# Kernel tuning notes

Hardware: AMD Instinct MI355X
Metric: run time of the kernel (lower is better)

## Reference

```python
import jax, jax.numpy as jnp
import numpy as np


def _conv(x, w, b, pad):
    y = jax.lax.conv_general_dilated(x, w, (1, 1), [(pad, pad), (pad, pad)],
                                     dimension_numbers=('NCHW', 'OIHW', 'NCHW'))
    return y + b[None, :, None, None]


def _leaky(x):
    return jnp.where(x >= 0, x, 0.2 * x)


def _up_nearest(t, s):
    return jnp.repeat(jnp.repeat(t, s, axis=2), s, axis=3)


def _to_plane(d, dx, dy, size):
    # nearest-upsample d,dx,dy by `size` and add per-subpixel plane offsets
    c = jnp.linspace(-(size - 1) / 2, (size - 1) / 2, size).astype(d.dtype)
    H, W = d.shape[2], d.shape[3]
    a = jnp.tile(c, W)[None, None, None, :]   # x-offset pattern along width
    b = jnp.tile(c, H)[None, None, :, None]   # y-offset pattern along height
    return _up_nearest(d, size) + a * _up_nearest(dx, size) + b * _up_nearest(dy, size)


def _warp(x, disp):
    # grid_sample(x, grid) with grid = (xx - disp, yy), align_corners=True, zero padding.
    # y coords are exact integers, so this reduces to 1-D linear interp along W.
    B, C, H, W = x.shape
    ix = jnp.arange(W, dtype=x.dtype)[None, None, :] - disp[:, 0]  # [B,H,W]
    x0 = jnp.floor(ix)
    wx = ix - x0
    x0i = x0.astype(jnp.int32)
    x1i = x0i + 1
    ok0 = ((x0i >= 0) & (x0i < W)).astype(x.dtype)
    ok1 = ((x1i >= 0) & (x1i < W)).astype(x.dtype)

    def gather(idx):
        idx = jnp.clip(idx, 0, W - 1)
        return jnp.take_along_axis(x, jnp.broadcast_to(idx[:, None], (B, C, H, W)), axis=3)

    return ((1 - wx) * ok0)[:, None] * gather(x0i) + (wx * ok1)[:, None] * gather(x1i)


def _unshuffle(x, r=4):
    B, C, H, W = x.shape
    return x.reshape(B, C, H // r, r, W // r, r).transpose(0, 1, 3, 5, 2, 4).reshape(B, C * r * r, H // r, W // r)


def _tile_warping(tile_plane, fea_l, fea_r):
    d, dx, dy = tile_plane[:, 0:1], tile_plane[:, 1:2], tile_plane[:, 2:3]
    cvs = []
    for k in (-1.0, 0.0, 1.0):
        local_d = _to_plane(d + k, dx, dy, 4)
        cv = jnp.sum(jnp.abs(fea_l - _warp(fea_r, local_d)), axis=1, keepdims=True)
        cvs.append(_unshuffle(cv, 4))
    return jnp.concatenate(cvs, axis=1)


def _upsample_hyp(h, scale=2.0, size=2):
    d = _to_plane(h[:, 0:1], h[:, 1:2], h[:, 2:3], size) * scale
    rest = _up_nearest(h[:, 1:], size)
    return jnp.concatenate([d, rest], axis=1)


def _forward(fea_l, fea_r, cur, prev,
             w_dec, b_dec, w0, b0,
             w_r0c1, b_r0c1, w_r0c2, b_r0c2,
             w_r1c1, b_r1c1, w_r1c2, b_r1c2,
             w_last, b_last):
    fea = _unshuffle(jnp.sum(jnp.abs(fea_l), axis=1, keepdims=True), 4)  # [B,16,H/4,W/4]

    cur_cv = _tile_warping(cur[:, :3], fea_l, fea_r)
    cur_cv = _leaky(_conv(jnp.concatenate([fea, cur_cv], 1), w_dec, b_dec, 0))

    up_prev = _upsample_hyp(prev, 2.0, 2)
    prev_cv = _tile_warping(up_prev[:, :3], fea_l, fea_r)
    prev_cv = _leaky(_conv(jnp.concatenate([fea, prev_cv], 1), w_dec, b_dec, 0))

    aug = jnp.concatenate([cur, cur_cv, up_prev, prev_cv], 1)  # 64 ch
    h = _leaky(_conv(aug, w0, b0, 0))
    # resblock0 (BasicBlock + outer LeakyReLU)
    t = _leaky(_conv(h, w_r0c1, b_r0c1, 1))
    h = _leaky(_conv(t, w_r0c2, b_r0c2, 1) + h)
    # resblock1
    t = _leaky(_conv(h, w_r1c1, b_r1c1, 1))
    h = _leaky(_conv(t, w_r1c2, b_r1c2, 1) + h)
    u = _conv(h, w_last, b_last, 1)  # 34 ch

    conf = u[:, :2]
    prev_delta = u[:, 2:18]
    cur_delta = u[:, 18:34]
    mask = jnp.argmax(conf, axis=1, keepdims=True).astype(u.dtype)

    upd_cur = cur + cur_delta
    upd_cur = jnp.concatenate([jax.nn.relu(upd_cur[:, :1]), upd_cur[:, 1:]], 1)
    upd_prev = up_prev + prev_delta
    upd_prev = jnp.concatenate([jax.nn.relu(upd_prev[:, :1]), upd_prev[:, 1:]], 1)

    refined = mask * upd_cur + (1 - mask) * upd_prev
    return (refined,
            jnp.concatenate([upd_cur, conf[:, 1:2]], 1),
            jnp.concatenate([upd_prev, conf[:, :1]], 1))


def setup_inputs() -> dict:
    key = jax.random.key(0)
    ks = jax.random.split(key, 16)
    B, C, H, W = 2, 16, 384, 1280
    Ht, Wt = H // 4, W // 4
    inp = {
        'fea_l': jax.random.normal(ks[0], (B, C, H, W), jnp.float32),
        'fea_r': jax.random.normal(ks[1], (B, C, H, W), jnp.float32),
        'current_hypothesis': jax.random.uniform(ks[2], (B, 16, Ht, Wt), jnp.float32) * 4.0,
        'prev_hypothesis': jax.random.uniform(ks[3], (B, 16, Ht // 2, Wt // 2), jnp.float32) * 4.0,
    }
    s = 0.05
    inp['w_dec'] = jax.random.normal(ks[4], (16, 64, 1, 1), jnp.float32) * s
    inp['b_dec'] = jax.random.normal(ks[5], (16,), jnp.float32) * s
    inp['w0'] = jax.random.normal(ks[6], (32, 64, 1, 1), jnp.float32) * s
    inp['b0'] = jax.random.normal(ks[7], (32,), jnp.float32) * s
    inp['w_r0c1'] = jax.random.normal(ks[8], (32, 32, 3, 3), jnp.float32) * s
    inp['b_r0c1'] = jax.random.normal(ks[9], (32,), jnp.float32) * s
    inp['w_r0c2'] = jax.random.normal(ks[10], (32, 32, 3, 3), jnp.float32) * s
    inp['b_r0c2'] = jax.random.normal(ks[11], (32,), jnp.float32) * s
    inp['w_r1c1'] = jax.random.normal(ks[12], (32, 32, 3, 3), jnp.float32) * s
    inp['b_r1c1'] = jax.random.normal(ks[13], (32,), jnp.float32) * s
    inp['w_r1c2'] = jax.random.normal(ks[14], (32, 32, 3, 3), jnp.float32) * s
    inp['b_r1c2'] = jax.random.normal(ks[15], (32,), jnp.float32) * s
    k2 = jax.random.split(jax.random.key(1), 2)
    inp['w_last'] = jax.random.normal(k2[0], (34, 32, 3, 3), jnp.float32) * s
    inp['b_last'] = jax.random.normal(k2[1], (34,), jnp.float32) * s
    return inp


def reference(fea_l, fea_r, current_hypothesis, prev_hypothesis,
              w_dec, b_dec, w0, b0,
              w_r0c1, b_r0c1, w_r0c2, b_r0c2,
              w_r1c1, b_r1c1, w_r1c2, b_r1c2,
              w_last, b_last):
    return _forward(fea_l, fea_r, current_hypothesis, prev_hypothesis,
                    w_dec, b_dec, w0, b0,
                    w_r0c1, b_r0c1, w_r0c2, b_r0c2,
                    w_r1c1, b_r1c1, w_r1c2, b_r1c2,
                    w_last, b_last)
```

## Files before the change

kernel.cpp:

```cpp
#include <hip/hip_runtime.h>
#include <hip/hip_bf16.h>

#define B_ 2
#define C_ 16
#define H_ 384
#define W_ 1280
#define HT_ 96
#define WT_ 320
#define SP_ (HT_*WT_)
#define NPIX_ (B_*SP_)
#define HP_ 48
#define WP_ 160
#define SPP_ (HP_*WP_)

__device__ __forceinline__ float leaky(float v){ return v >= 0.f ? v : 0.2f*v; }

__global__ __launch_bounds__(256) void k_sentinel(float* __restrict__ out, int n, float v){
    int i = blockIdx.x*256 + threadIdx.x;
    if (i < n) out[i] = v;
}

__global__ __launch_bounds__(256) void k_warpfused(const float* __restrict__ cur,
        const float* __restrict__ prev,
        const float* __restrict__ fl, const float* __restrict__ fr,
        const float* __restrict__ wdec, const float* __restrict__ bdec,
        float* __restrict__ outc, float* __restrict__ outp){
    __shared__ float vc[16][65];
    __shared__ float vp[16][49];
    __shared__ float wl[64][16];
    int tid = threadIdx.x;
    for (int i = tid; i < 1024; i += 256) wl[i>>4][i&15] = wdec[(i&15)*64 + (i>>4)];

    int tp  = tid >> 4;
    int sub = tid & 15;
    int yy = sub >> 2, xx = sub & 3;
    int ty = blockIdx.y;
    int tx = blockIdx.x*16 + tp;
    int b  = blockIdx.z;
    int y = ty*4 + yy, x = tx*4 + xx;

    size_t cb = ((size_t)(b*16)*HT_ + ty)*WT_ + tx;
    float dC  = cur[cb];
    float dxC = cur[cb + SP_];
    float dyC = cur[cb + 2*SP_];
    size_t pb = ((size_t)(b*16)*HP_ + (ty>>1))*WP_ + (tx>>1);
    float pd  = prev[pb];
    float pdx = prev[pb + SPP_];
    float pdy = prev[pb + 2*SPP_];
    float cxs = (tx & 1) ? 0.5f : -0.5f;
    float cys = (ty & 1) ? 0.5f : -0.5f;
    float dP  = (pd + cxs*pdx + cys*pdy) * 2.0f;

    const float c4[4] = {-1.5f,-0.5f,0.5f,1.5f};
    float ld0C = dC + c4[xx]*dxC + c4[yy]*dyC;
    float ld0P = dP + c4[xx]*pdx + c4[yy]*pdy;

    float wloC[4], whiC[4]; int xcC[4];
    {
        float ix  = (float)x - ld0C;
        float x0f = floorf(ix);
        float wx  = ix - x0f;
        int   x0  = (int)x0f;
        #pragma unroll
        for (int j = 0; j < 4; j++){
            int xi = x0 + (j-1);
            bool ok = (xi >= 0) && (xi < W_);
            xcC[j]  = xi < 0 ? 0 : (xi > W_-1 ? W_-1 : xi);
            wloC[j] = ok ? (1.f - wx) : 0.f;
            whiC[j] = ok ? wx : 0.f;
        }
    }
    float wloP[4], whiP[4]; int xcP[4];
    {
        float ix  = (float)x - ld0P;
        float x0f = floorf(ix);
        float wx  = ix - x0f;
        int   x0  = (int)x0f;
        #pragma unroll
        for (int j = 0; j < 4; j++){
            int xi = x0 + (j-1);
            bool ok = (xi >= 0) && (xi < W_);
            xcP[j]  = xi < 0 ? 0 : (xi > W_-1 ? W_-1 : xi);
            wloP[j] = ok ? (1.f - wx) : 0.f;
            whiP[j] = ok ? wx : 0.f;
        }
    }
    const float* plc = fl + (size_t)(b*C_)*H_*W_ + (size_t)y*W_ + x;
    const float* prr = fr + (size_t)(b*C_)*H_*W_ + (size_t)y*W_;
    float fsum=0.f, s0C=0.f, s1C=0.f, s2C=0.f, s0P=0.f, s1P=0.f, s2P=0.f;
    #pragma unroll 4
    for (int c = 0; c < C_; c++){
        const float* prc = prr + (size_t)c*H_*W_;
        float a  = plc[(size_t)c*H_*W_];
        float c0 = prc[xcC[0]];
        float c1 = prc[xcC[1]];
        float c2 = prc[xcC[2]];
        float c3 = prc[xcC[3]];
        float p0 = prc[xcP[0]];
        float p1 = prc[xcP[1]];
        float p2 = prc[xcP[2]];
        float p3 = prc[xcP[3]];
        fsum += fabsf(a);
        s0C += fabsf(a - (wloC[2]*c2 + whiC[3]*c3));
        s1C += fabsf(a - (wloC[1]*c1 + whiC[2]*c2));
        s2C += fabsf(a - (wloC[0]*c0 + whiC[1]*c1));
        s0P += fabsf(a - (wloP[2]*p2 + whiP[3]*p3));
        s1P += fabsf(a - (wloP[1]*p1 + whiP[2]*p2));
        s2P += fabsf(a - (wloP[0]*p0 + whiP[1]*p1));
    }
    vc[tp][sub]      = fsum;
    vc[tp][16 + sub] = s0C;
    vc[tp][32 + sub] = s1C;
    vc[tp][48 + sub] = s2C;
    vp[tp][sub]      = s0P;
    vp[tp][16 + sub] = s1P;
    vp[tp][32 + sub] = s2P;
    __syncthreads();
    int oc  = tid >> 4;
    int tp2 = tid & 15;
    float common = 0.f, aC = 0.f, aP = 0.f;
    #pragma unroll 8
    for (int ic = 0; ic < 16; ic++) common += vc[tp2][ic] * wl[ic][oc];
    #pragma unroll 8
    for (int ic = 16; ic < 64; ic++){
        aC += vc[tp2][ic]      * wl[ic][oc];
        aP += vp[tp2][ic - 16] * wl[ic][oc];
    }
    float bb = bdec[oc];
    size_t ob = ((size_t)(b*16 + oc)*HT_ + ty)*WT_ + blockIdx.x*16 + tp2;
    outc[ob] = leaky(common + aC + bb);
    outp[ob] = leaky(common + aP + bb);
}

__global__ __launch_bounds__(256) void k_conv0(const float* __restrict__ cur,
        const float* __restrict__ ccv, const float* __restrict__ prev,
        const float* __restrict__ pcv, const float* __restrict__ w,
        const float* __restrict__ bias, float* __restrict__ out){
    __shared__ float wl[64][32];
    __shared__ float bl[32];
    int tid = threadIdx.x;
    for (int i = tid; i < 2048; i += 256) wl[i>>5][i&31] = w[(i&31)*64 + (i>>5)];
    if (tid < 32) bl[tid] = bias[tid];
    __syncthreads();
    int idx = blockIdx.x*256 + tid;
    int b = idx / SP_, sp = idx % SP_;
    int y = sp / WT_, x = sp % WT_;
    float acc[32];
    #pragma unroll
    for (int o = 0; o < 32; o++) acc[o] = 0.f;
    const float* p0 = cur + (size_t)b*16*SP_ + sp;
    #pragma unroll 2
    for (int i = 0; i < 16; i++){
        float v = p0[(size_t)i*SP_];
        #pragma unroll
        for (int o = 0; o < 32; o++) acc[o] += v*wl[i][o];
    }
    const float* p1 = ccv + (size_t)b*16*SP_ + sp;
    #pragma unroll 2
    for (int i = 0; i < 16; i++){
        float v = p1[(size_t)i*SP_];
        #pragma unroll
        for (int o = 0; o < 32; o++) acc[o] += v*wl[16+i][o];
    }
    size_t src = ((size_t)(b*16)*HP_ + (y>>1))*WP_ + (x>>1);
    {
        float pd  = prev[src];
        float pdx = prev[src + SPP_];
        float pdy = prev[src + 2*SPP_];
        float cx = (x & 1) ? 0.5f : -0.5f;
        float cy = (y & 1) ? 0.5f : -0.5f;
        float v = (pd + cx*pdx + cy*pdy) * 2.0f;
        #pragma unroll
        for (int o = 0; o < 32; o++) acc[o] += v*wl[32][o];
    }
    #pragma unroll 2
    for (int i = 1; i < 16; i++){
        float v = prev[src + (size_t)i*SPP_];
        #pragma unroll
        for (int o = 0; o < 32; o++) acc[o] += v*wl[32+i][o];
    }
    const float* p3 = pcv + (size_t)b*16*SP_ + sp;
    #pragma unroll 2
    for (int i = 0; i < 16; i++){
        float v = p3[(size_t)i*SP_];
        #pragma unroll
        for (int o = 0; o < 32; o++) acc[o] += v*wl[48+i][o];
    }
    float* po = out + (size_t)b*32*SP_ + sp;
    #pragma unroll
    for (int o = 0; o < 32; o++) po[(size_t)o*SP_] = leaky(acc[o] + bl[o]);
}

template<bool RES>
__global__ __launch_bounds__(256) void k_conv3(const float* __restrict__ in,
        const float* __restrict__ w, const float* __restrict__ bias,
        const float* res, float* out){
    __shared__ float it[8][6][34];
    __shared__ float wl[8][9][32];
    int tid = threadIdx.x;
    int gx = blockIdx.x*32, gy = blockIdx.y*4;
    int b = blockIdx.z;
    int ocg  = tid >> 5;
    int slot = tid & 31;
    int tx4  = (slot & 7)*4;
    int ty   = slot >> 3;
    float acc[4][4];
    #pragma unroll
    for (int o = 0; o < 4; o++)
        #pragma unroll
        for (int p = 0; p < 4; p++) acc[o][p] = 0.f;

    for (int ic0 = 0; ic0 < 32; ic0 += 8){
        for (int i = tid; i < 8*6*34; i += 256){
            int ic = i/(6*34); int r = i - ic*(6*34);
            int iy = r/34;     int ixx = r - iy*34;
            int ggy = gy + iy - 1, ggx = gx + ixx - 1;
            float v = 0.f;
            if (ggy >= 0 && ggy < HT_ && ggx >= 0 && ggx < WT_)
                v = in[((size_t)(b*32 + ic0+ic)*HT_ + ggy)*WT_ + ggx];
            it[ic][iy][ixx] = v;
        }
        for (int i = tid; i < 2304; i += 256){
            int ic = i/288; int r = i - ic*288;
            int kk = r >> 5; int oc = r & 31;
            wl[ic][kk][oc] = w[(size_t)(oc*32 + ic0+ic)*9 + kk];
        }
        __syncthreads();
        #pragma unroll
        for (int ic = 0; ic < 8; ic++){
            #pragma unroll
            for (int dy = 0; dy < 3; dy++){
                float inr[6];
                #pragma unroll
                for (int j = 0; j < 6; j++) inr[j] = it[ic][ty+dy][tx4+j];
                #pragma unroll
                for (int dx = 0; dx < 3; dx++){
                    const float4 wv = *(const float4*)(&wl[ic][dy*3+dx][ocg*4]);
                    const float wa[4] = {wv.x, wv.y, wv.z, wv.w};
                    #pragma unroll
                    for (int o = 0; o < 4; o++)
                        #pragma unroll
                        for (int p = 0; p < 4; p++)
                            acc[o][p] += inr[dx+p]*wa[o];
                }
            }
        }
        __syncthreads();
    }
    int oc0 = ocg*4;
    int yo = gy + ty;
    #pragma unroll
    for (int o = 0; o < 4; o++){
        float bo = bias[oc0+o];
        size_t ob = ((size_t)(b*32 + oc0+o)*HT_ + yo)*WT_ + gx + tx4;
        #pragma unroll
        for (int p = 0; p < 4; p++){
            float v = acc[o][p] + bo;
            if (RES) v += res[ob+p];
            out[ob+p] = leaky(v);
        }
    }
}

__global__ __launch_bounds__(256) void k_last(const float* __restrict__ in,
        const float* __restrict__ w, const float* __restrict__ bias,
        const float* __restrict__ cur, const float* __restrict__ prev,
        float* __restrict__ out){
    __shared__ float it[8][10][34];
    __shared__ float wl[8][9][36];
    __shared__ float bl[34];
    int tid = threadIdx.x;
    int gx = blockIdx.x*32, gy = blockIdx.y*8;
    int b = blockIdx.z;
    int tx = tid & 31, ty = tid >> 5;
    if (tid < 34) bl[tid] = bias[tid];
    float acc[34];
    #pragma unroll
    for (int o = 0; o < 34; o++) acc[o] = 0.f;

    for (int ic0 = 0; ic0 < 32; ic0 += 8){
        for (int i = tid; i < 8*10*34; i += 256){
            int ic = i/340; int r = i - ic*340;
            int iy = r/34;  int ixx = r - iy*34;
            int ggy = gy + iy - 1, ggx = gx + ixx - 1;
            float v = 0.f;
            if (ggy >= 0 && ggy < HT_ && ggx >= 0 && ggx < WT_)
                v = in[((size_t)(b*32 + ic0+ic)*HT_ + ggy)*WT_ + ggx];
            it[ic][iy][ixx] = v;
        }
        for (int i = tid; i < 8*9*34; i += 256){
            int ic = i/306; int r = i - ic*306;
            int kk = r/34;  int oc = r - kk*34;
            wl[ic][kk][oc] = w[(size_t)(oc*32 + ic0+ic)*9 + kk];
        }
        __syncthreads();
        for (int ic = 0; ic < 8; ic++){
            #pragma unroll
            for (int dy = 0; dy < 3; dy++){
                const float vv[3] = { it[ic][ty+dy][tx], it[ic][ty+dy][tx+1], it[ic][ty+dy][tx+2] };
                #pragma unroll
                for (int dx = 0; dx < 3; dx++){
                    const float* wp = &wl[ic][dy*3+dx][0];
                    float v = vv[dx];
                    #pragma unroll
                    for (int o = 0; o < 34; o++) acc[o] += v*wp[o];
                }
            }
        }
        __syncthreads();
    }
    int x = gx + tx, y = gy + ty;
    size_t pix = (size_t)y*WT_ + x;
    float conf0 = acc[0] + bl[0];
    float conf1 = acc[1] + bl[1];
    bool m = conf1 > conf0;
    size_t src = ((size_t)(b*16)*HP_ + (y>>1))*WP_ + (x>>1);
    float cx = (x & 1) ? 0.5f : -0.5f;
    float cy = (y & 1) ? 0.5f : -0.5f;
    const float* cp = cur + (size_t)b*16*SP_ + pix;
    float* o0 = out +               (size_t)b*16*SP_ + pix;
    float* o1 = out +  983040u  +   (size_t)b*17*SP_ + pix;
    float* o2 = out + 2027520u  +   (size_t)b*17*SP_ + pix;
    #pragma unroll
    for (int c = 0; c < 16; c++){
        float upv;
        if (c == 0){
            float dv  = prev[src];
            float dxv = prev[src + SPP_];
            float dyv = prev[src + 2*SPP_];
            upv = (dv + cx*dxv + cy*dyv) * 2.0f;
        } else {
            upv = prev[src + (size_t)c*SPP_];
        }
        float ucv = cp[(size_t)c*SP_] + acc[18+c] + bl[18+c];
        upv = upv + acc[2+c] + bl[2+c];
        if (c == 0){ ucv = fmaxf(ucv, 0.f); upv = fmaxf(upv, 0.f); }
        float rf = m ? ucv : upv;
        o0[(size_t)c*SP_] = rf;
        o1[(size_t)c*SP_] = ucv;
        o2[(size_t)c*SP_] = upv;
    }
    o1[(size_t)16*SP_] = conf1;
    o2[(size_t)16*SP_] = conf0;
}

#define WS_NEED (32u*NPIX_*4u)
#define OUT_ELEMS 3072000

extern "C" void kernel_launch(void* const* d_in, const int* in_sizes, int n_in,
                              void* d_out, int out_size, void* d_ws, size_t ws_size,
                              hipStream_t stream) {
    const float* fea_l  = (const float*)d_in[0];
    const float* fea_r  = (const float*)d_in[1];
    const float* cur    = (const float*)d_in[2];
    const float* prev   = (const float*)d_in[3];
    const float* w_dec  = (const float*)d_in[4];
    const float* b_dec  = (const float*)d_in[5];
    const float* w0     = (const float*)d_in[6];
    const float* b0     = (const float*)d_in[7];
    const float* w_r0c1 = (const float*)d_in[8];
    const float* b_r0c1 = (const float*)d_in[9];
    const float* w_r0c2 = (const float*)d_in[10];
    const float* b_r0c2 = (const float*)d_in[11];
    const float* w_r1c1 = (const float*)d_in[12];
    const float* b_r1c1 = (const float*)d_in[13];
    const float* w_r1c2 = (const float*)d_in[14];
    const float* b_r1c2 = (const float*)d_in[15];
    const float* w_last = (const float*)d_in[16];
    const float* b_last = (const float*)d_in[17];

    float* out = (float*)d_out;

    if (ws_size < (size_t)WS_NEED){
        k_sentinel<<<(OUT_ELEMS+255)/256, 256, 0, stream>>>(out, OUT_ELEMS, (float)(ws_size >> 10));
        return;
    }

    float* h = (float*)d_ws;
    float* curcv  = out;
    float* prevcv = out + 983040;
    float* t      = out;

    dim3 gw(20, 96, 2);
    k_warpfused<<<gw, 256, 0, stream>>>(cur, prev, fea_l, fea_r, w_dec, b_dec, curcv, prevcv);

    k_conv0<<<240, 256, 0, stream>>>(cur, curcv, prev, prevcv, w0, b0, h);

    dim3 g3(10, 24, 2);
    k_conv3<false><<<g3, 256, 0, stream>>>(h, w_r0c1, b_r0c1, nullptr, t);
    k_conv3<true> <<<g3, 256, 0, stream>>>(t, w_r0c2, b_r0c2, h, h);
    k_conv3<false><<<g3, 256, 0, stream>>>(h, w_r1c1, b_r1c1, nullptr, t);
    k_conv3<true> <<<g3, 256, 0, stream>>>(t, w_r1c2, b_r1c2, h, h);

    dim3 gl(10, 12, 2);
    k_last<<<gl, 256, 0, stream>>>(h, w_last, b_last, cur, prev, out);
}
```

Baseline: 476.4 us.

## Fuse conv0 into warp cost-volume kernel and split conv3 output channels across blocks

The 1x1 conv0 is folded into the warp/cost-volume kernel. Its 64 input channels (cur, cost volume, upsampled prev, prev cost volume) are staged in shared memory, and the result is written straight to h. This drops the global write and reread of the two intermediate cost-volume tensors and one kernel launch. Separately, the 3x3 conv kernel now splits its 32 output channels into two halves across grid z and computes 2 pixels per thread instead of 4. That doubles block count for more parallelism but reloads the input tile twice.

```diff
diff --git a/kernel.cpp b/kernel.cpp
--- a/kernel.cpp
+++ b/kernel.cpp
@@ -24,20 +24,46 @@
         const float* __restrict__ prev,
         const float* __restrict__ fl, const float* __restrict__ fr,
         const float* __restrict__ wdec, const float* __restrict__ bdec,
-        float* __restrict__ outc, float* __restrict__ outp){
+        const float* __restrict__ w0, const float* __restrict__ b0,
+        float* __restrict__ h){
     __shared__ float vc[16][65];
     __shared__ float vp[16][49];
     __shared__ float wl[64][16];
+    __shared__ float inb[16][65];
+    __shared__ float w0l[64][33];
+    __shared__ float bl0[32];
     int tid = threadIdx.x;
     for (int i = tid; i < 1024; i += 256) wl[i>>4][i&15] = wdec[(i&15)*64 + (i>>4)];
+    for (int i = tid; i < 2048; i += 256) w0l[i>>5][i&31] = w0[(i&31)*64 + (i>>5)];
+    if (tid < 32) bl0[tid] = b0[tid];
 
     int tp  = tid >> 4;
     int sub = tid & 15;
     int yy = sub >> 2, xx = sub & 3;
     int ty = blockIdx.y;
-    int tx = blockIdx.x*16 + tp;
+    int tx0 = blockIdx.x*16;
+    int tx = tx0 + tp;
     int b  = blockIdx.z;
     int y = ty*4 + yy, x = tx*4 + xx;
+
+    {
+        int ch = tid >> 4, px = tid & 15;
+        int txp = tx0 + px;
+        inb[px][ch] = cur[((size_t)(b*16 + ch)*HT_ + ty)*WT_ + txp];
+        size_t pbase = ((size_t)(b*16)*HP_ + (ty>>1))*WP_ + (txp>>1);
+        float v;
+        if (ch == 0){
+            float dv  = prev[pbase];
+            float dxv = prev[pbase + SPP_];
+            float dyv = prev[pbase + 2*SPP_];
+            float cxs = (txp & 1) ? 0.5f : -0.5f;
+            float cys = (ty  & 1) ? 0.5f : -0.5f;
+            v = (dv + cxs*dxv + cys*dyv) * 2.0f;
+        } else {
+            v = prev[pbase + (size_t)ch*SPP_];
+        }
+        inb[px][32 + ch] = v;
+    }
 
     size_t cb = ((size_t)(b*16)*HT_ + ty)*WT_ + tx;
     float dC  = cur[cb];
@@ -116,79 +142,39 @@
     vp[tp][16 + sub] = s1P;
     vp[tp][32 + sub] = s2P;
     __syncthreads();
-    int oc  = tid >> 4;
-    int tp2 = tid & 15;
-    float common = 0.f, aC = 0.f, aP = 0.f;
-    #pragma unroll 8
-    for (int ic = 0; ic < 16; ic++) common += vc[tp2][ic] * wl[ic][oc];
-    #pragma unroll 8
-    for (int ic = 16; ic < 64; ic++){
-        aC += vc[tp2][ic]      * wl[ic][oc];
-        aP += vp[tp2][ic - 16] * wl[ic][oc];
-    }
-    float bb = bdec[oc];
-    size_t ob = ((size_t)(b*16 + oc)*HT_ + ty)*WT_ + blockIdx.x*16 + tp2;
-    outc[ob] = leaky(common + aC + bb);
-    outp[ob] = leaky(common + aP + bb);
-}
-
-__global__ __launch_bounds__(256) void k_conv0(const float* __restrict__ cur,
-        const float* __restrict__ ccv, const float* __restrict__ prev,
-        const float* __restrict__ pcv, const float* __restrict__ w,
-        const float* __restrict__ bias, float* __restrict__ out){
-    __shared__ float wl[64][32];
-    __shared__ float bl[32];
-    int tid = threadIdx.x;
-    for (int i = tid; i < 2048; i += 256) wl[i>>5][i&31] = w[(i&31)*64 + (i>>5)];
-    if (tid < 32) bl[tid] = bias[tid];
+
+    {
+        int oc  = tid >> 4;
+        int tp2 = tid & 15;
+        float common = 0.f, aC = 0.f, aP = 0.f;
+        #pragma unroll 8
+        for (int ic = 0; ic < 16; ic++) common += vc[tp2][ic] * wl[ic][oc];
+        #pragma unroll 8
+        for (int ic = 16; ic < 64; ic++){
+            aC += vc[tp2][ic]      * wl[ic][oc];
+            aP += vp[tp2][ic - 16] * wl[ic][oc];
+        }
+        float bb = bdec[oc];
+        inb[tp2][16 + oc] = leaky(common + aC + bb);
+        inb[tp2][48 + oc] = leaky(common + aP + bb);
+    }
     __syncthreads();
-    int idx = blockIdx.x*256 + tid;
-    int b = idx / SP_, sp = idx % SP_;
-    int y = sp / WT_, x = sp % WT_;
-    float acc[32];
-    #pragma unroll
-    for (int o = 0; o < 32; o++) acc[o] = 0.f;
-    const float* p0 = cur + (size_t)b*16*SP_ + sp;
-    #pragma unroll 2
-    for (int i = 0; i < 16; i++){
-        float v = p0[(size_t)i*SP_];
-        #pragma unroll
-        for (int o = 0; o < 32; o++) acc[o] += v*wl[i][o];
-    }
-    const float* p1 = ccv + (size_t)b*16*SP_ + sp;
-    #pragma unroll 2
-    for (int i = 0; i < 16; i++){
-        float v = p1[(size_t)i*SP_];
-        #pragma unroll
-        for (int o = 0; o < 32; o++) acc[o] += v*wl[16+i][o];
-    }
-    size_t src = ((size_t)(b*16)*HP_ + (y>>1))*WP_ + (x>>1);
-    {
-        float pd  = prev[src];
-        float pdx = prev[src + SPP_];
-        float pdy = prev[src + 2*SPP_];
-        float cx = (x & 1) ? 0.5f : -0.5f;
-        float cy = (y & 1) ? 0.5f : -0.5f;
-        float v = (pd + cx*pdx + cy*pdy) * 2.0f;
-        #pragma unroll
-        for (int o = 0; o < 32; o++) acc[o] += v*wl[32][o];
-    }
-    #pragma unroll 2
-    for (int i = 1; i < 16; i++){
-        float v = prev[src + (size_t)i*SPP_];
-        #pragma unroll
-        for (int o = 0; o < 32; o++) acc[o] += v*wl[32+i][o];
-    }
-    const float* p3 = pcv + (size_t)b*16*SP_ + sp;
-    #pragma unroll 2
-    for (int i = 0; i < 16; i++){
-        float v = p3[(size_t)i*SP_];
-        #pragma unroll
-        for (int o = 0; o < 32; o++) acc[o] += v*wl[48+i][o];
-    }
-    float* po = out + (size_t)b*32*SP_ + sp;
-    #pragma unroll
-    for (int o = 0; o < 32; o++) po[(size_t)o*SP_] = leaky(acc[o] + bl[o]);
+
+    {
+        int og = tid >> 4;
+        int px = tid & 15;
+        float acc0 = bl0[og];
+        float acc1 = bl0[og + 16];
+        #pragma unroll 8
+        for (int ic = 0; ic < 64; ic++){
+            float v = inb[px][ic];
+            acc0 += v * w0l[ic][og];
+            acc1 += v * w0l[ic][og + 16];
+        }
+        size_t hb = ((size_t)(b*32 + og)*HT_ + ty)*WT_ + tx0 + px;
+        h[hb]              = leaky(acc0);
+        h[hb + (size_t)16*HT_*WT_] = leaky(acc1);
+    }
 }
 
 template<bool RES>
@@ -196,19 +182,20 @@
         const float* __restrict__ w, const float* __restrict__ bias,
         const float* res, float* out){
     __shared__ float it[8][6][34];
-    __shared__ float wl[8][9][32];
+    __shared__ float wl[8][9][16];
     int tid = threadIdx.x;
     int gx = blockIdx.x*32, gy = blockIdx.y*4;
-    int b = blockIdx.z;
-    int ocg  = tid >> 5;
-    int slot = tid & 31;
-    int tx4  = (slot & 7)*4;
-    int ty   = slot >> 3;
-    float acc[4][4];
+    int b     = blockIdx.z >> 1;
+    int ocsel = blockIdx.z & 1;
+    int ocg  = tid >> 6;
+    int slot = tid & 63;
+    int tx2  = (slot & 15)*2;
+    int ty   = slot >> 4;
+    float acc[4][2];
     #pragma unroll
     for (int o = 0; o < 4; o++)
         #pragma unroll
-        for (int p = 0; p < 4; p++) acc[o][p] = 0.f;
+        for (int p = 0; p < 2; p++) acc[o][p] = 0.f;
 
     for (int ic0 = 0; ic0 < 32; ic0 += 8){
         for (int i = tid; i < 8*6*34; i += 256){
@@ -220,19 +207,19 @@
                 v = in[((size_t)(b*32 + ic0+ic)*HT_ + ggy)*WT_ + ggx];
             it[ic][iy][ixx] = v;
         }
-        for (int i = tid; i < 2304; i += 256){
-            int ic = i/288; int r = i - ic*288;
-            int kk = r >> 5; int oc = r & 31;
-            wl[ic][kk][oc] = w[(size_t)(oc*32 + ic0+ic)*9 + kk];
+        for (int i = tid; i < 1152; i += 256){
+            int ic = i/144; int r = i - ic*144;
+            int kk = r >> 4; int ocl = r & 15;
+            wl[ic][kk][ocl] = w[(size_t)((ocsel*16 + ocl)*32 + ic0+ic)*9 + kk];
         }
         __syncthreads();
         #pragma unroll
         for (int ic = 0; ic < 8; ic++){
             #pragma unroll
             for (int dy = 0; dy < 3; dy++){
-                float inr[6];
+                float inr[4];
                 #pragma unroll
-                for (int j = 0; j < 6; j++) inr[j] = it[ic][ty+dy][tx4+j];
+                for (int j = 0; j < 4; j++) inr[j] = it[ic][ty+dy][tx2+j];
                 #pragma unroll
                 for (int dx = 0; dx < 3; dx++){
                     const float4 wv = *(const float4*)(&wl[ic][dy*3+dx][ocg*4]);
@@ -240,21 +227,21 @@
                     #pragma unroll
                     for (int o = 0; o < 4; o++)
                         #pragma unroll
-                        for (int p = 0; p < 4; p++)
+                        for (int p = 0; p < 2; p++)
                             acc[o][p] += inr[dx+p]*wa[o];
                 }
             }
         }
         __syncthreads();
     }
-    int oc0 = ocg*4;
+    int oc0 = ocsel*16 + ocg*4;
     int yo = gy + ty;
     #pragma unroll
     for (int o = 0; o < 4; o++){
         float bo = bias[oc0+o];
-        size_t ob = ((size_t)(b*32 + oc0+o)*HT_ + yo)*WT_ + gx + tx4;
-        #pragma unroll
-        for (int p = 0; p < 4; p++){
+        size_t ob = ((size_t)(b*32 + oc0+o)*HT_ + yo)*WT_ + gx + tx2;
+        #pragma unroll
+        for (int p = 0; p < 2; p++){
             float v = acc[o][p] + bo;
             if (RES) v += res[ob+p];
             out[ob+p] = leaky(v);
@@ -377,16 +364,12 @@
     }
 
     float* h = (float*)d_ws;
-    float* curcv  = out;
-    float* prevcv = out + 983040;
-    float* t      = out;
+    float* t = out;
 
     dim3 gw(20, 96, 2);
-    k_warpfused<<<gw, 256, 0, stream>>>(cur, prev, fea_l, fea_r, w_dec, b_dec, curcv, prevcv);
-
-    k_conv0<<<240, 256, 0, stream>>>(cur, curcv, prev, prevcv, w0, b0, h);
-
-    dim3 g3(10, 24, 2);
+    k_warpfused<<<gw, 256, 0, stream>>>(cur, prev, fea_l, fea_r, w_dec, b_dec, w0, b0, h);
+
+    dim3 g3(10, 24, 4);
     k_conv3<false><<<g3, 256, 0, stream>>>(h, w_r0c1, b_r0c1, nullptr, t);
     k_conv3<true> <<<g3, 256, 0, stream>>>(t, w_r0c2, b_r0c2, h, h);
     k_conv3<false><<<g3, 256, 0, stream>>>(h, w_r1c1, b_r1c1, nullptr, t);
```

Result: faster. 453.7 us (-4.8%).
